# Performance work log

Measured on AMD Instinct MI355X. Metric: run time of the kernel, lower is better.

Reference implementation:

```python
import jax, jax.numpy as jnp
import numpy as np

BATCH = 64
DIM_IN = 4096
DIM_OUT = 4096


def setup_inputs() -> dict:
    key = jax.random.key(0)
    kx, km, kt = jax.random.split(key, 3)
    x = jax.random.bernoulli(kx, 0.5, (BATCH, DIM_IN))                      # bool [B, dim_in]
    masks = jax.random.bernoulli(km, 0.5, (DIM_IN, DIM_OUT))                # bool [dim_in, dim_out]
    thresholds = jax.random.randint(kt, (DIM_OUT,), 0, DIM_IN, dtype=jnp.int32)  # int [dim_out]
    return {"x": x, "masks": masks, "thresholds": thresholds}


def reference(x, masks, thresholds):
    # sum_i XNOR(x_i, m_ij) = #(both true) + #(both false)
    #                       = dim_in - sum_i x_i - sum_i m_ij + 2 * (x @ m)
    # This reproduces the broadcast-XNOR + reduce-sum math exactly without
    # materializing the [B, dim_in, dim_out] boolean tensor.
    xi = x.astype(jnp.int32)
    mi = masks.astype(jnp.int32)
    both_true = jnp.einsum('bi,io->bo', xi, mi)                             # int32 [B, dim_out]
    sums = DIM_IN - xi.sum(axis=1, keepdims=True) - mi.sum(axis=0, keepdims=True) + 2 * both_true
    return sums > thresholds[None, :]                                       # bool [B, dim_out]
```

## Files before the change

kernel.cpp:

```cpp
#include <hip/hip_runtime.h>
#include <stdint.h>

#define DIM_IN  4096
#define DIM_OUT 4096
#define BATCH   64

typedef unsigned long long u64;
typedef uint32_t u32;

__device__ __forceinline__ bool is_word_fmt(const u32* __restrict__ p) {
    bool words = true;
#pragma unroll
    for (int i = 0; i < 8; ++i) {
        u32 v = p[i];
        if (v > 1u && v != 0x3F800000u) words = false;
    }
    return words;
}

__global__ __launch_bounds__(256) void pack_kernel(
        const void* __restrict__ masks, const void* __restrict__ x,
        u64* __restrict__ mp, u64* __restrict__ xp) {
    const int bid = blockIdx.x;
    if (bid < 1024) {
        const bool words = is_word_fmt((const u32*)masks);
        const int wid = bid * 4 + (threadIdx.x >> 6);
        const int w   = wid >> 6;
        const int o   = ((wid & 63) << 6) + (threadIdx.x & 63);
        const int row0 = w * 64;

        u64 bits = 0;
        if (words) {
            const u32* pw = (const u32*)masks + (size_t)row0 * DIM_OUT + o;
#pragma unroll
            for (int rb = 0; rb < 4; ++rb) {
                u32 v[16];
#pragma unroll
                for (int r = 0; r < 16; ++r)
                    v[r] = pw[(size_t)(rb * 16 + r) * DIM_OUT];
#pragma unroll
                for (int r = 0; r < 16; ++r)
                    bits |= (u64)(v[r] != 0u) << (rb * 16 + r);
            }
        } else {
            const uint8_t* pb = (const uint8_t*)masks + (size_t)row0 * DIM_OUT + o;
#pragma unroll
            for (int rb = 0; rb < 4; ++rb) {
                uint8_t v[16];
#pragma unroll
                for (int r = 0; r < 16; ++r)
                    v[r] = pb[(size_t)(rb * 16 + r) * DIM_OUT];
#pragma unroll
                for (int r = 0; r < 16; ++r)
                    bits |= (u64)(v[r] != 0u) << (rb * 16 + r);
            }
        }
        mp[(size_t)w * DIM_OUT + o] = bits;
    } else {
        const bool words = is_word_fmt((const u32*)x);
        const int bxid = bid - 1024;
        const int wave = bxid * 4 + (threadIdx.x >> 6);
        const int lane = threadIdx.x & 63;
        const int base = wave * 64;

#pragma unroll 16
        for (int k = 0; k < 64; ++k) {
            const int idx = base + k;
            const size_t e = (size_t)idx * 64 + lane;
            bool pred;
            if (words) pred = ((const u32*)x)[e] != 0u;
            else       pred = ((const uint8_t*)x)[e] != 0u;
            const u64 m = __ballot(pred);
            if (lane == 0) xp[idx] = m;
        }
    }
}

__global__ __launch_bounds__(256) void bnn_kernel(
        const u64* __restrict__ mp, const u64* __restrict__ xp,
        const int* __restrict__ thr, int* __restrict__ out) {
    const int o  = blockIdx.x * 256 + threadIdx.x;
    const int b0 = blockIdx.y * 4;

    const u64* __restrict__ x0 = xp + (size_t)(b0 + 0) * 64;
    const u64* __restrict__ x1 = xp + (size_t)(b0 + 1) * 64;
    const u64* __restrict__ x2 = xp + (size_t)(b0 + 2) * 64;
    const u64* __restrict__ x3 = xp + (size_t)(b0 + 3) * 64;

    int a0 = 0, a1 = 0, a2 = 0, a3 = 0;
#pragma unroll 16
    for (int w = 0; w < 64; ++w) {
        const u64 mw = mp[(size_t)w * DIM_OUT + o];
        a0 += __popcll(x0[w] ^ mw);
        a1 += __popcll(x1[w] ^ mw);
        a2 += __popcll(x2[w] ^ mw);
        a3 += __popcll(x3[w] ^ mw);
    }

    const int t = thr[o];
    out[(size_t)(b0 + 0) * DIM_OUT + o] = (DIM_IN - a0) > t ? 1 : 0;
    out[(size_t)(b0 + 1) * DIM_OUT + o] = (DIM_IN - a1) > t ? 1 : 0;
    out[(size_t)(b0 + 2) * DIM_OUT + o] = (DIM_IN - a2) > t ? 1 : 0;
    out[(size_t)(b0 + 3) * DIM_OUT + o] = (DIM_IN - a3) > t ? 1 : 0;
}

extern "C" void kernel_launch(void* const* d_in, const int* in_sizes, int n_in,
                              void* d_out, int out_size, void* d_ws, size_t ws_size,
                              hipStream_t stream) {
    const void* x     = d_in[0];
    const void* masks = d_in[1];
    const int*  thr   = (const int*)d_in[2];
    int* out = (int*)d_out;

    u64* mp = (u64*)d_ws;
    u64* xp = (u64*)((char*)d_ws + (size_t)64 * DIM_OUT * 8);

    pack_kernel<<<dim3(1040), dim3(256), 0, stream>>>(masks, x, mp, xp);
    bnn_kernel<<<dim3(16, 16), dim3(256), 0, stream>>>(mp, xp, thr, out);
}
```

Baseline: 42.41 us.

## Fuse packing and popcount into one kernel with shared-memory bit tiles

Replaces the separate pack and XNOR-popcount kernels with one kernel. Each block packs a 16-column mask slice and the whole input x into shared memory, then computes outputs for all 64 batch rows. This removes the global workspace round trip and one kernel launch. The cost is that every block redundantly reads and packs all of x, the grid is smaller, and the mask reads are less coalesced.

Result: slower. 106.4 us (+150.9%).

```diff
diff --git a/kernel.cpp b/kernel.cpp
--- a/kernel.cpp
+++ b/kernel.cpp
@@ -18,90 +18,121 @@
     return words;
 }
 
-__global__ __launch_bounds__(256) void pack_kernel(
+__global__ __launch_bounds__(256) void fused1_kernel(
         const void* __restrict__ masks, const void* __restrict__ x,
-        u64* __restrict__ mp, u64* __restrict__ xp) {
-    const int bid = blockIdx.x;
-    if (bid < 1024) {
+        const int* __restrict__ thr, int* __restrict__ out) {
+    __shared__ u64 xp[64 * 64];
+    __shared__ u64 mpl[64 * 16];
+
+    const int tid  = threadIdx.x;
+    const int lane = tid & 63;
+    const int o0   = blockIdx.x * 16;
+
+    {
         const bool words = is_word_fmt((const u32*)masks);
-        const int wid = bid * 4 + (threadIdx.x >> 6);
-        const int w   = wid >> 6;
-        const int o   = ((wid & 63) << 6) + (threadIdx.x & 63);
-        const int row0 = w * 64;
+        const int c16 = tid & 15;
+        const int s   = tid >> 4;
+        u64 acc[4] = {0ull, 0ull, 0ull, 0ull};
 
-        u64 bits = 0;
         if (words) {
-            const u32* pw = (const u32*)masks + (size_t)row0 * DIM_OUT + o;
+            const u32* base = (const u32*)masks
+                            + (size_t)(s * 256) * DIM_OUT + o0 + c16;
 #pragma unroll
-            for (int rb = 0; rb < 4; ++rb) {
+            for (int rb = 0; rb < 16; ++rb) {
                 u32 v[16];
 #pragma unroll
-                for (int r = 0; r < 16; ++r)
-                    v[r] = pw[(size_t)(rb * 16 + r) * DIM_OUT];
+                for (int rr = 0; rr < 16; ++rr)
+                    v[rr] = base[(size_t)(rb * 16 + rr) * DIM_OUT];
 #pragma unroll
-                for (int r = 0; r < 16; ++r)
-                    bits |= (u64)(v[r] != 0u) << (rb * 16 + r);
+                for (int rr = 0; rr < 16; ++rr) {
+                    const int r = rb * 16 + rr;
+                    acc[r & 3] |= (u64)(v[rr] != 0u) << (r >> 2);
+                }
             }
         } else {
-            const uint8_t* pb = (const uint8_t*)masks + (size_t)row0 * DIM_OUT + o;
+            const uint8_t* base = (const uint8_t*)masks
+                                + (size_t)(s * 256) * DIM_OUT + o0 + c16;
 #pragma unroll
-            for (int rb = 0; rb < 4; ++rb) {
+            for (int rb = 0; rb < 16; ++rb) {
                 uint8_t v[16];
 #pragma unroll
-                for (int r = 0; r < 16; ++r)
-                    v[r] = pb[(size_t)(rb * 16 + r) * DIM_OUT];
+                for (int rr = 0; rr < 16; ++rr)
+                    v[rr] = base[(size_t)(rb * 16 + rr) * DIM_OUT];
 #pragma unroll
-                for (int r = 0; r < 16; ++r)
-                    bits |= (u64)(v[r] != 0u) << (rb * 16 + r);
+                for (int rr = 0; rr < 16; ++rr) {
+                    const int r = rb * 16 + rr;
+                    acc[r & 3] |= (u64)(v[rr] != 0u) << (r >> 2);
+                }
             }
         }
-        mp[(size_t)w * DIM_OUT + o] = bits;
-    } else {
-        const bool words = is_word_fmt((const u32*)x);
-        const int bxid = bid - 1024;
-        const int wave = bxid * 4 + (threadIdx.x >> 6);
-        const int lane = threadIdx.x & 63;
-        const int base = wave * 64;
+#pragma unroll
+        for (int cc = 0; cc < 4; ++cc)
+            mpl[(s * 4 + cc) * 16 + c16] = acc[cc];
+    }
 
-#pragma unroll 16
-        for (int k = 0; k < 64; ++k) {
-            const int idx = base + k;
-            const size_t e = (size_t)idx * 64 + lane;
-            bool pred;
-            if (words) pred = ((const u32*)x)[e] != 0u;
-            else       pred = ((const uint8_t*)x)[e] != 0u;
-            const u64 m = __ballot(pred);
-            if (lane == 0) xp[idx] = m;
+    {
+        const bool xwords = is_word_fmt((const u32*)x);
+        const int wv = tid >> 6;
+        if (xwords) {
+            const uint4* src = (const uint4*)x;
+#pragma unroll 8
+            for (int k = 0; k < 256; ++k) {
+                const int B = wv * 256 + k;
+                const uint4 v = src[(size_t)B * 64 + lane];
+                const u64 b0 = __ballot(v.x != 0u);
+                const u64 b1 = __ballot(v.y != 0u);
+                const u64 b2 = __ballot(v.z != 0u);
+                const u64 b3 = __ballot(v.w != 0u);
+                if (lane < 4) {
+                    const u64 bb = lane == 0 ? b0 : lane == 1 ? b1
+                                 : lane == 2 ? b2 : b3;
+                    xp[B * 4 + lane] = bb;
+                }
+            }
+        } else {
+            const u32* src = (const u32*)x;
+#pragma unroll 8
+            for (int k = 0; k < 256; ++k) {
+                const int B = wv * 256 + k;
+                const u32 v = src[(size_t)B * 64 + lane];
+                const u64 b0 = __ballot((v & 0x000000FFu) != 0u);
+                const u64 b1 = __ballot((v & 0x0000FF00u) != 0u);
+                const u64 b2 = __ballot((v & 0x00FF0000u) != 0u);
+                const u64 b3 = __ballot((v & 0xFF000000u) != 0u);
+                if (lane < 4) {
+                    const u64 bb = lane == 0 ? b0 : lane == 1 ? b1
+                                 : lane == 2 ? b2 : b3;
+                    xp[B * 4 + lane] = bb;
+                }
+            }
         }
     }
-}
 
-__global__ __launch_bounds__(256) void bnn_kernel(
-        const u64* __restrict__ mp, const u64* __restrict__ xp,
-        const int* __restrict__ thr, int* __restrict__ out) {
-    const int o  = blockIdx.x * 256 + threadIdx.x;
-    const int b0 = blockIdx.y * 4;
+    __syncthreads();
 
-    const u64* __restrict__ x0 = xp + (size_t)(b0 + 0) * 64;
-    const u64* __restrict__ x1 = xp + (size_t)(b0 + 1) * 64;
-    const u64* __restrict__ x2 = xp + (size_t)(b0 + 2) * 64;
-    const u64* __restrict__ x3 = xp + (size_t)(b0 + 3) * 64;
+    {
+        const int c16 = tid & 15;
+        const int bq  = tid >> 4;
+        const int o   = o0 + c16;
+        const int t   = thr[o];
 
-    int a0 = 0, a1 = 0, a2 = 0, a3 = 0;
-#pragma unroll 16
-    for (int w = 0; w < 64; ++w) {
-        const u64 mw = mp[(size_t)w * DIM_OUT + o];
-        a0 += __popcll(x0[w] ^ mw);
-        a1 += __popcll(x1[w] ^ mw);
-        a2 += __popcll(x2[w] ^ mw);
-        a3 += __popcll(x3[w] ^ mw);
+        int a[4] = {0, 0, 0, 0};
+#pragma unroll 4
+        for (int gc = 0; gc < 64; ++gc) {
+            const u64 m = mpl[gc * 16 + c16];
+            const int g = gc >> 2, cc = gc & 3;
+#pragma unroll
+            for (int j = 0; j < 4; ++j) {
+                const int b = bq * 4 + j;
+                a[j] += __popcll(xp[(b * 16 + g) * 4 + cc] ^ m);
+            }
+        }
+#pragma unroll
+        for (int j = 0; j < 4; ++j) {
+            const int b = bq * 4 + j;
+            out[(size_t)b * DIM_OUT + o] = (DIM_IN - a[j]) > t ? 1 : 0;
+        }
     }
-
-    const int t = thr[o];
-    out[(size_t)(b0 + 0) * DIM_OUT + o] = (DIM_IN - a0) > t ? 1 : 0;
-    out[(size_t)(b0 + 1) * DIM_OUT + o] = (DIM_IN - a1) > t ? 1 : 0;
-    out[(size_t)(b0 + 2) * DIM_OUT + o] = (DIM_IN - a2) > t ? 1 : 0;
-    out[(size_t)(b0 + 3) * DIM_OUT + o] = (DIM_IN - a3) > t ? 1 : 0;
 }
 
 extern "C" void kernel_launch(void* const* d_in, const int* in_sizes, int n_in,
@@ -112,9 +143,5 @@
     const int*  thr   = (const int*)d_in[2];
     int* out = (int*)d_out;
 
-    u64* mp = (u64*)d_ws;
-    u64* xp = (u64*)((char*)d_ws + (size_t)64 * DIM_OUT * 8);
-
-    pack_kernel<<<dim3(1040), dim3(256), 0, stream>>>(masks, x, mp, xp);
-    bnn_kernel<<<dim3(16, 16), dim3(256), 0, stream>>>(mp, xp, thr, out);
+    fused1_kernel<<<dim3(256), dim3(256), 0, stream>>>(masks, x, thr, out);
 }
```

## Stage mask tiles into LDS via direct global-to-LDS 16-byte loads before bit packing

Applied to the files above, without the earlier changes.

The mask-packing path now has each block load a 64x256 word tile straight into shared memory with 16-byte global_load_lds transfers, then builds each 64-bit column word from LDS. Previously every thread issued 64 scalar strided 4-byte loads. The aim is wider, better-coalesced global reads and more bytes in flight. The cost is 64KB of LDS per block, which caps occupancy and is also reserved by the x-packing blocks, plus an added barrier.

New measurement: 42.90 us. About the same (+1.1%).

```diff
diff --git a/kernel.cpp b/kernel.cpp
--- a/kernel.cpp
+++ b/kernel.cpp
@@ -18,58 +18,71 @@
     return words;
 }
 
+__device__ __forceinline__ void gl_lds16(const u32* g, u32* l) {
+    __builtin_amdgcn_global_load_lds(
+        (const __attribute__((address_space(1))) u32*)g,
+        (__attribute__((address_space(3))) u32*)l, 16, 0, 0);
+}
+
 __global__ __launch_bounds__(256) void pack_kernel(
         const void* __restrict__ masks, const void* __restrict__ x,
         u64* __restrict__ mp, u64* __restrict__ xp) {
-    const int bid = blockIdx.x;
+    __shared__ u32 tile[64 * 256];
+    const int bid  = blockIdx.x;
+    const int tid  = threadIdx.x;
+    const int lane = tid & 63;
+
     if (bid < 1024) {
         const bool words = is_word_fmt((const u32*)masks);
-        const int wid = bid * 4 + (threadIdx.x >> 6);
-        const int w   = wid >> 6;
-        const int o   = ((wid & 63) << 6) + (threadIdx.x & 63);
+        const int w    = bid >> 4;
+        const int oseg = bid & 15;
+        const int o0   = oseg * 256;
         const int row0 = w * 64;
 
-        u64 bits = 0;
         if (words) {
-            const u32* pw = (const u32*)masks + (size_t)row0 * DIM_OUT + o;
+            const int wv = tid >> 6;
+            const u32* gbase = (const u32*)masks
+                             + (size_t)row0 * DIM_OUT + o0 + lane * 4;
 #pragma unroll
-            for (int rb = 0; rb < 4; ++rb) {
-                u32 v[16];
+            for (int k = 0; k < 16; ++k) {
+                const int r = wv * 16 + k;
+                gl_lds16(gbase + (size_t)r * DIM_OUT, &tile[r * 256]);
+            }
+            asm volatile("s_waitcnt vmcnt(0)" ::: "memory");
+            __syncthreads();
+
+            u32 lo = 0, hi = 0;
 #pragma unroll
-                for (int r = 0; r < 16; ++r)
-                    v[r] = pw[(size_t)(rb * 16 + r) * DIM_OUT];
+            for (int r = 0; r < 32; ++r)
+                lo |= (u32)(tile[r * 256 + tid] != 0u) << r;
 #pragma unroll
-                for (int r = 0; r < 16; ++r)
-                    bits |= (u64)(v[r] != 0u) << (rb * 16 + r);
-            }
+            for (int r = 32; r < 64; ++r)
+                hi |= (u32)(tile[r * 256 + tid] != 0u) << (r - 32);
+            mp[(size_t)w * DIM_OUT + o0 + tid] = (u64)lo | ((u64)hi << 32);
         } else {
-            const uint8_t* pb = (const uint8_t*)masks + (size_t)row0 * DIM_OUT + o;
+            const uint8_t* base = (const uint8_t*)masks
+                                + (size_t)row0 * DIM_OUT + o0 + tid;
+            u32 lo = 0, hi = 0;
 #pragma unroll
-            for (int rb = 0; rb < 4; ++rb) {
-                uint8_t v[16];
+            for (int r = 0; r < 32; ++r)
+                lo |= (u32)(base[(size_t)r * DIM_OUT] != 0u) << r;
 #pragma unroll
-                for (int r = 0; r < 16; ++r)
-                    v[r] = pb[(size_t)(rb * 16 + r) * DIM_OUT];
-#pragma unroll
-                for (int r = 0; r < 16; ++r)
-                    bits |= (u64)(v[r] != 0u) << (rb * 16 + r);
-            }
+            for (int r = 32; r < 64; ++r)
+                hi |= (u32)(base[(size_t)r * DIM_OUT] != 0u) << (r - 32);
+            mp[(size_t)w * DIM_OUT + o0 + tid] = (u64)lo | ((u64)hi << 32);
         }
-        mp[(size_t)w * DIM_OUT + o] = bits;
     } else {
-        const bool words = is_word_fmt((const u32*)x);
+        const bool xwords = is_word_fmt((const u32*)x);
         const int bxid = bid - 1024;
-        const int wave = bxid * 4 + (threadIdx.x >> 6);
-        const int lane = threadIdx.x & 63;
+        const int wave = bxid * 4 + (tid >> 6);
         const int base = wave * 64;
-
 #pragma unroll 16
         for (int k = 0; k < 64; ++k) {
             const int idx = base + k;
             const size_t e = (size_t)idx * 64 + lane;
             bool pred;
-            if (words) pred = ((const u32*)x)[e] != 0u;
-            else       pred = ((const uint8_t*)x)[e] != 0u;
+            if (xwords) pred = ((const u32*)x)[e] != 0u;
+            else        pred = ((const uint8_t*)x)[e] != 0u;
             const u64 m = __ballot(pred);
             if (lane == 0) xp[idx] = m;
         }
@@ -113,7 +126,7 @@
     int* out = (int*)d_out;
 
     u64* mp = (u64*)d_ws;
-    u64* xp = (u64*)((char*)d_ws + (size_t)64 * DIM_OUT * 8);
+    u64* xp = (u64*)((char*)d_ws + (size_t)2 * 1024 * 1024);
 
     pack_kernel<<<dim3(1040), dim3(256), 0, stream>>>(masks, x, mp, xp);
     bnn_kernel<<<dim3(16, 16), dim3(256), 0, stream>>>(mp, xp, thr, out);
```
